# Optimization experiments

Measured on AMD Instinct MI355X. Metric: run time of the kernel, lower is better.

The kernel has to match this reference:

```python
import jax, jax.numpy as jnp
import numpy as np

N = 32768          # flattened vectors
HALF = 256         # each input half
D = 512            # embedding_dim
K = 2048           # num_embeddings
COMMITMENT_COST = 0.25


def setup_inputs() -> dict:
    key = jax.random.key(0)
    k0, k1, kw, kb, ke = jax.random.split(key, 5)
    x0 = jax.random.normal(k0, (N, HALF), dtype=jnp.float32)
    x1 = jax.random.normal(k1, (N, HALF), dtype=jnp.float32)
    # pre_lin: nn.Linear(D, D) -> weight [D, D], bias [D]
    lim = 1.0 / np.sqrt(D)
    W = jax.random.uniform(kw, (D, D), minval=-lim, maxval=lim, dtype=jnp.float32)
    b = jax.random.uniform(kb, (D,), minval=-lim, maxval=lim, dtype=jnp.float32)
    # codebook: embedding.weight.data.normal_()
    emb = jax.random.normal(ke, (K, D), dtype=jnp.float32)
    return {"x0": x0, "x1": x1, "W": W, "b": b, "emb": emb}


def reference(x0, x1, W, b, emb):
    # hstack the two halves -> [N, D]
    inputs = jnp.concatenate([x0, x1], axis=1)
    h = inputs @ W.T + b                       # pre_lin, [N, D]
    # squared L2 distances to codebook, [N, K]
    d2 = (jnp.sum(h * h, axis=1, keepdims=True)
          + jnp.sum(emb * emb, axis=1)
          - 2.0 * (h @ emb.T))
    idx = jnp.argmin(d2, axis=1)               # [N]
    encodings = jax.nn.one_hot(idx, emb.shape[0], dtype=jnp.float32)  # [N, K]
    quantized = emb[idx]                       # gather == one_hot @ emb, [N, D]
    # commitment loss (eval mode: no EMA update)
    e_latent_loss = jnp.mean((jax.lax.stop_gradient(quantized) - h) ** 2)
    loss = COMMITMENT_COST * e_latent_loss
    # straight-through estimator
    q_st = h + jax.lax.stop_gradient(quantized - h)
    avg_probs = jnp.mean(encodings, axis=0)
    perplexity = jnp.exp(-jnp.sum(avg_probs * jnp.log(avg_probs + 1e-10)))
    # row-major reshape [N, D] -> [2, N, D/2], as in torch.reshape
    q_out = jnp.reshape(q_st, (2, q_st.shape[0], -1))
    return loss, q_out, perplexity, encodings
```

## Files before the change

kernel.cpp:

```cpp
#include <hip/hip_runtime.h>
#include <cfloat>
#include <cmath>

#define NROWS 32768
#define DDIM  512
#define KCODES 2048

#define OUT_Q    1
#define OUT_PERP 16777217
#define OUT_ENC  16777218

#define AP_OFF    16777216
#define BP_OFF    33554432
#define XS_OFF    34603008
#define WS_OFF    51380224
#define ENORM_OFF 51642368
#define PVAL_OFF  51644416
#define PSEC_OFF  52692992
#define PIDX_OFF  53741568
#define AG_OFF    54790144
#define PVAL2_OFF 63178752
#define PSEC2_OFF 63703040
#define PIDX2_OFF 64227328
#define RB_OFF    64751616
#define RI_OFF    64784384

#define CAP1 16384
#define CAP2 4096
#define EPS1 0.32f
#define EPS2 0.02f

typedef __attribute__((ext_vector_type(8))) short  bf16x8;
typedef __attribute__((ext_vector_type(4))) float  f32x4;

__device__ __forceinline__ unsigned short f2bf(float f) {
  unsigned u = __float_as_uint(f);
  unsigned r = (u + 0x7FFF + ((u >> 16) & 1)) >> 16;
  return (unsigned short)r;
}
__device__ __forceinline__ float bf2f(unsigned short h) {
  return __uint_as_float(((unsigned)h) << 16);
}
__device__ __forceinline__ void gload16(const void* g, void* l) {
  __builtin_amdgcn_global_load_lds(
      (const __attribute__((address_space(1))) unsigned int*)g,
      (__attribute__((address_space(3))) unsigned int*)l, 16, 0, 0);
}
__device__ __forceinline__ ushort4 hi4(float4 v) {
  return make_ushort4(f2bf(v.x), f2bf(v.y), f2bf(v.z), f2bf(v.w));
}
__device__ __forceinline__ ushort4 lo4(float4 v, ushort4 h) {
  return make_ushort4(f2bf(v.x - bf2f(h.x)), f2bf(v.y - bf2f(h.y)),
                      f2bf(v.z - bf2f(h.z)), f2bf(v.w - bf2f(h.w)));
}

template<int TERMS, int KSTEPS>
__device__ __forceinline__ void kloop64(const unsigned short* __restrict__ Am,
    const unsigned short* __restrict__ Bm, short* Asm, short* Bsm,
    f32x4 (&acc)[4][4], int t, int wr, int wc, int lr, int lg) {
  for (int kt = 0; kt < KSTEPS; ++kt) {
    const int ph = kt >> 3, r64 = (kt & 7) * 64;
    int koffA, koffB;
    if (TERMS == 1)      { koffA = r64;                          koffB = r64; }
    else if (TERMS == 3) { koffA = (ph == 1) ? 512 + r64 : r64;  koffB = (ph == 2) ? 512 + r64 : r64; }
    else                 { koffA = (ph & 1) ? 512 + r64 : r64;   koffB = (ph & 2) ? 512 + r64 : r64; }
    const unsigned short* Agp = Am + koffA;
    const unsigned short* Bgp = Bm + koffB;
#pragma unroll
    for (int i = 0; i < 4; ++i) {
      const int chunk = i * 256 + t;
      const int r = chunk >> 3;
      const int c8s = (chunk & 7) ^ (r & 7);
      gload16(Agp + (size_t)r * 1024 + c8s * 8, Asm + chunk * 8);
      gload16(Bgp + (size_t)r * 1024 + c8s * 8, Bsm + chunk * 8);
    }
    __syncthreads();
#pragma unroll
    for (int kk = 0; kk < 2; ++kk) {
      const int xk = (kk * 32 + lg * 8) ^ ((lr & 7) << 3);
      bf16x8 a[4], b[4];
#pragma unroll
      for (int mi = 0; mi < 4; ++mi)
        a[mi] = *(const bf16x8*)&Asm[(wr * 64 + mi * 16 + lr) * 64 + xk];
#pragma unroll
      for (int ni = 0; ni < 4; ++ni)
        b[ni] = *(const bf16x8*)&Bsm[(wc * 64 + ni * 16 + lr) * 64 + xk];
#pragma unroll
      for (int mi = 0; mi < 4; ++mi)
#pragma unroll
        for (int ni = 0; ni < 4; ++ni)
          acc[mi][ni] = __builtin_amdgcn_mfma_f32_16x16x32_bf16(a[mi], b[ni], acc[mi][ni], 0, 0, 0);
    }
    __syncthreads();
  }
}

__global__ __launch_bounds__(256) void kprep_x(const float* __restrict__ x0,
    const float* __restrict__ x1, const float* __restrict__ W,
    unsigned short* __restrict__ Xs, unsigned short* __restrict__ Ws,
    unsigned int* __restrict__ wsclr) {
  if (blockIdx.x == 16640) {
    for (int i = threadIdx.x; i < 2052; i += 256) wsclr[i] = 0u;
    return;
  }
  const int i = blockIdx.x * 256 + threadIdx.x;
  if (i < 4194304) {
    const int half = i >> 21;
    const int j = i & 2097151;
    const int n = j >> 6;
    const int c4 = (j & 63) * 4;
    const float* src = half ? x1 : x0;
    const float4 v = *(const float4*)&src[(size_t)n * 256 + c4];
    const ushort4 hh = hi4(v);
    unsigned short* row = Xs + (size_t)n * 1024 + half * 256;
    *(ushort4*)&row[c4]       = hh;
    *(ushort4*)&row[512 + c4] = lo4(v, hh);
  } else {
    const int j = i - 4194304;
    const int r = j >> 7;
    const int c4 = (j & 127) * 4;
    const float4 v = *(const float4*)&W[(size_t)r * 512 + c4];
    const ushort4 hh = hi4(v);
    unsigned short* row = Ws + (size_t)r * 1024;
    *(ushort4*)&row[c4]       = hh;
    *(ushort4*)&row[512 + c4] = lo4(v, hh);
  }
}

__global__ __launch_bounds__(256) void kprep_emb(const float* __restrict__ emb,
    unsigned short* __restrict__ Bp, float* __restrict__ enorms) {
  __shared__ float part[4];
  const int t = threadIdx.x;
  const int row = blockIdx.x * 2 + (t >> 7);
  const int c4 = (t & 127) * 4;
  const float4 v = *(const float4*)&emb[(size_t)row * 512 + c4];
  const ushort4 hh = hi4(v);
  unsigned short* brow = Bp + (size_t)row * 1024;
  *(ushort4*)&brow[c4]       = hh;
  *(ushort4*)&brow[512 + c4] = lo4(v, hh);
  float s = v.x * v.x + v.y * v.y + v.z * v.z + v.w * v.w;
#pragma unroll
  for (int off = 32; off > 0; off >>= 1) s += __shfl_down(s, off);
  if ((t & 63) == 0) part[t >> 6] = s;
  __syncthreads();
  if (t == 0)   enorms[row] = part[0] + part[1];
  if (t == 128) enorms[row] = part[2] + part[3];
}

__global__ __launch_bounds__(256) void kgemm1_mfma(
    const unsigned short* __restrict__ Xs, const unsigned short* __restrict__ Ws,
    const float* __restrict__ bias, unsigned short* __restrict__ Ap) {
  __shared__ short Asm[128 * 64];
  __shared__ short Bsm[128 * 64];
  const int bid = blockIdx.x;
  const int n = (bid >> 3) & 3;
  const int m = (bid & 7) * 32 + (bid >> 5);
  const int m0 = m * 128, j0 = n * 128;
  const int t = threadIdx.x;
  const int wid = t >> 6, wr = wid >> 1, wc = wid & 1;
  const int lr = t & 15, lg = (t >> 4) & 3;

  f32x4 acc[4][4];
#pragma unroll
  for (int mi = 0; mi < 4; ++mi)
#pragma unroll
    for (int ni = 0; ni < 4; ++ni) acc[mi][ni] = (f32x4){0.f, 0.f, 0.f, 0.f};

  kloop64<4, 32>(Xs + (size_t)m0 * 1024, Ws + (size_t)j0 * 1024,
                 Asm, Bsm, acc, t, wr, wc, lr, lg);

#pragma unroll
  for (int ni = 0; ni < 4; ++ni) {
    const int col = j0 + wc * 64 + ni * 16 + lr;
    const float bb = bias[col];
#pragma unroll
    for (int mi = 0; mi < 4; ++mi)
#pragma unroll
      for (int jj = 0; jj < 4; ++jj) {
        const int row = m0 + wr * 64 + mi * 16 + lg * 4 + jj;
        const float v = acc[mi][ni][jj] + bb;
        const unsigned short hb = f2bf(v);
        Ap[(size_t)row * 1024 + col]       = hb;
        Ap[(size_t)row * 1024 + 512 + col] = f2bf(v - bf2f(hb));
      }
  }
}

template<int TERMS, bool GATED>
__global__ __launch_bounds__(256) void kdist_t(
    const unsigned short* __restrict__ A, const unsigned short* __restrict__ B,
    const float* __restrict__ enorms, float* __restrict__ pval,
    float* __restrict__ psec, int* __restrict__ pidx,
    const int* __restrict__ nflag, int mrows) {
  __shared__ short Asm[128 * 64];
  __shared__ short Bsm[128 * 64];
  const int bid = blockIdx.x;
  int m, n;
  if (GATED) {
    m = bid >> 4;
    n = bid & 15;
    const int nf = min(*nflag, CAP1);
    if (m >= ((nf + 127) >> 7)) return;
  } else {
    m = (bid & 7) * 32 + (bid >> 7);
    n = (bid >> 3) & 15;
  }
  const int m0 = m * 128;
  const int n0 = n * 128;
  const int t = threadIdx.x;
  const int wid = t >> 6, wr = wid >> 1, wc = wid & 1;
  const int lr = t & 15, lg = (t >> 4) & 3;

  f32x4 acc[4][4];
#pragma unroll
  for (int mi = 0; mi < 4; ++mi)
#pragma unroll
    for (int ni = 0; ni < 4; ++ni) acc[mi][ni] = (f32x4){0.f, 0.f, 0.f, 0.f};

  kloop64<TERMS, TERMS * 8>(A + (size_t)m0 * 1024, B + (size_t)n0 * 1024,
                            Asm, Bsm, acc, t, wr, wc, lr, lg);

  float en[4]; int kb[4];
#pragma unroll
  for (int ni = 0; ni < 4; ++ni) {
    kb[ni] = n0 + wc * 64 + ni * 16 + lr;
    en[ni] = enorms[kb[ni]];
  }
  const int p = n * 2 + wc;
#pragma unroll
  for (int mi = 0; mi < 4; ++mi)
#pragma unroll
    for (int j = 0; j < 4; ++j) {
      float bv = fmaf(-2.f, acc[mi][0][j], en[0]);
      int bk = kb[0];
      float sv = FLT_MAX;
#pragma unroll
      for (int ni = 1; ni < 4; ++ni) {
        const float v = fmaf(-2.f, acc[mi][ni][j], en[ni]);
        if (v < bv) { sv = bv; bv = v; bk = kb[ni]; }
        else sv = fminf(sv, v);
      }
#pragma unroll
      for (int msk = 1; msk < 16; msk <<= 1) {
        const float ob = __shfl_xor(bv, msk);
        const int   ok = __shfl_xor(bk, msk);
        const float os = __shfl_xor(sv, msk);
        if (ob < bv || (ob == bv && ok < bk)) { sv = fminf(bv, os); bv = ob; bk = ok; }
        else sv = fminf(sv, ob);
      }
      if (lr == 0) {
        const int row = m0 + wr * 64 + mi * 16 + lg * 4 + j;
        pval[(size_t)p * mrows + row] = bv;
        psec[(size_t)p * mrows + row] = sv;
        pidx[(size_t)p * mrows + row] = bk;
      }
    }
}

__global__ __launch_bounds__(256) void kreduce(const float* __restrict__ pval,
    const float* __restrict__ psec, const int* __restrict__ pidx,
    int* __restrict__ idx, int* __restrict__ nflag, int* __restrict__ flags) {
  const int r = blockIdx.x * 256 + threadIdx.x;
  float bv = FLT_MAX, sv = FLT_MAX;
  int bk = 0;
#pragma unroll
  for (int p = 0; p < 32; ++p) {
    const float v1 = pval[p * NROWS + r];
    const int   k1 = pidx[p * NROWS + r];
    const float s1 = psec[p * NROWS + r];
    if (v1 < bv || (v1 == bv && k1 < bk)) { sv = fminf(bv, s1); bv = v1; bk = k1; }
    else sv = fminf(sv, v1);
  }
  idx[r] = bk;
  if (sv - bv < EPS1) {
    const int pos = atomicAdd(nflag, 1);
    if (pos < CAP1) flags[pos] = r;
  }
}

__global__ __launch_bounds__(256) void kgather(const unsigned short* __restrict__ Ap,
    const int* __restrict__ flags, const int* __restrict__ nflag,
    unsigned short* __restrict__ Ag) {
  const int nf = min(*nflag, CAP1);
  const int t = threadIdx.x;
  const int g8 = blockIdx.x;
  for (int i = t; i < 8 * 256; i += 256) {
    const int rr = i >> 8;
    const int g = g8 * 8 + rr;
    if (g < nf) {
      const int c = i & 255;
      ((ushort4*)(Ag + (size_t)g * 1024))[c] =
          ((const ushort4*)(Ap + (size_t)flags[g] * 1024))[c];
    }
  }
}

__global__ __launch_bounds__(256) void kreduce2(const float* __restrict__ pval2,
    const float* __restrict__ psec2, const int* __restrict__ pidx2,
    const int* __restrict__ flags, const int* __restrict__ nflag,
    int* __restrict__ idx, int* __restrict__ nflag2, int* __restrict__ flags2) {
  const int nf = min(*nflag, CAP1);
  const int g = blockIdx.x * 256 + threadIdx.x;
  if (g >= nf) return;
  float bv = FLT_MAX, sv = FLT_MAX;
  int bk = 0;
#pragma unroll
  for (int p = 0; p < 32; ++p) {
    const float v1 = pval2[p * CAP1 + g];
    const int   k1 = pidx2[p * CAP1 + g];
    const float s1 = psec2[p * CAP1 + g];
    if (v1 < bv || (v1 == bv && k1 < bk)) { sv = fminf(bv, s1); bv = v1; bk = k1; }
    else sv = fminf(sv, v1);
  }
  const int r = flags[g];
  if (sv - bv >= EPS2) {
    idx[r] = bk;
  } else {
    const int pos = atomicAdd(nflag2, 1);
    if (pos < CAP2) flags2[pos] = r;
  }
}

__global__ __launch_bounds__(256) void krescore_p(
    const unsigned short* __restrict__ Ap, const float* __restrict__ emb,
    const float* __restrict__ enorms, const int* __restrict__ flags2,
    const int* __restrict__ nflag2, float* __restrict__ rbest,
    int* __restrict__ rbidx) {
  const int nf2 = min(*nflag2, CAP2);
  const int g2 = blockIdx.x >> 3;
  if (g2 >= nf2) return;
  const int chunk = blockIdx.x & 7;
  const int t = threadIdx.x;
  const int r = flags2[g2];
  __shared__ float hr[512];
  __shared__ float rv[256];
  __shared__ int   rk[256];
  for (int i = t; i < 128; i += 256) {
    const ushort4 hh = *(const ushort4*)&Ap[(size_t)r * 1024 + i * 4];
    const ushort4 ll = *(const ushort4*)&Ap[(size_t)r * 1024 + 512 + i * 4];
    hr[i * 4 + 0] = bf2f(hh.x) + bf2f(ll.x);
    hr[i * 4 + 1] = bf2f(hh.y) + bf2f(ll.y);
    hr[i * 4 + 2] = bf2f(hh.z) + bf2f(ll.z);
    hr[i * 4 + 3] = bf2f(hh.w) + bf2f(ll.w);
  }
  __syncthreads();
  const int c = chunk * 256 + t;
  const float* er = emb + (size_t)c * 512;
  float d0 = 0.f, d1 = 0.f, d2 = 0.f, d3 = 0.f;
#pragma unroll 8
  for (int dd = 0; dd < 512; dd += 16) {
    const float4 e0 = *(const float4*)&er[dd];
    const float4 e1 = *(const float4*)&er[dd + 4];
    const float4 e2 = *(const float4*)&er[dd + 8];
    const float4 e3 = *(const float4*)&er[dd + 12];
    d0 = fmaf(hr[dd+0],  e0.x, d0); d0 = fmaf(hr[dd+1],  e0.y, d0);
    d0 = fmaf(hr[dd+2],  e0.z, d0); d0 = fmaf(hr[dd+3],  e0.w, d0);
    d1 = fmaf(hr[dd+4],  e1.x, d1); d1 = fmaf(hr[dd+5],  e1.y, d1);
    d1 = fmaf(hr[dd+6],  e1.z, d1); d1 = fmaf(hr[dd+7],  e1.w, d1);
    d2 = fmaf(hr[dd+8],  e2.x, d2); d2 = fmaf(hr[dd+9],  e2.y, d2);
    d2 = fmaf(hr[dd+10], e2.z, d2); d2 = fmaf(hr[dd+11], e2.w, d2);
    d3 = fmaf(hr[dd+12], e3.x, d3); d3 = fmaf(hr[dd+13], e3.y, d3);
    d3 = fmaf(hr[dd+14], e3.z, d3); d3 = fmaf(hr[dd+15], e3.w, d3);
  }
  const float dot = (d0 + d1) + (d2 + d3);
  rv[t] = fmaf(-2.f, dot, enorms[c]);
  rk[t] = c;
  __syncthreads();
  for (int off = 128; off > 0; off >>= 1) {
    if (t < off) {
      const float v2 = rv[t + off];
      const int   k2 = rk[t + off];
      if (v2 < rv[t] || (v2 == rv[t] && k2 < rk[t])) { rv[t] = v2; rk[t] = k2; }
    }
    __syncthreads();
  }
  if (t == 0) {
    rbest[g2 * 8 + chunk] = rv[0];
    rbidx[g2 * 8 + chunk] = rk[0];
  }
}

__global__ __launch_bounds__(256) void kpick(const float* __restrict__ rbest,
    const int* __restrict__ rbidx, const int* __restrict__ flags2,
    const int* __restrict__ nflag2, int* __restrict__ idx) {
  const int g2 = blockIdx.x * 256 + threadIdx.x;
  if (g2 >= min(*nflag2, CAP2)) return;
  float bv = rbest[g2 * 8];
  int   bk = rbidx[g2 * 8];
#pragma unroll
  for (int c = 1; c < 8; ++c) {
    const float v = rbest[g2 * 8 + c];
    const int   k = rbidx[g2 * 8 + c];
    if (v < bv || (v == bv && k < bk)) { bv = v; bk = k; }
  }
  idx[flags2[g2]] = bk;
}

__global__ __launch_bounds__(256) void kquant(const unsigned short* __restrict__ Ap,
    const float* __restrict__ emb, const int* __restrict__ idx,
    float* __restrict__ qout, double* __restrict__ partials,
    int* __restrict__ counts) {
  const int t = threadIdx.x;
  const int base = blockIdx.x * 256 + t;
  float ls = 0.f;
#pragma unroll
  for (int i = 0; i < 8; ++i) {
    const int f4 = base + i * 524288;
    const int n  = f4 >> 7;
    const int c4 = (f4 & 127) << 2;
    const int in = idx[n];
    const ushort4 hh = *(const ushort4*)&Ap[(size_t)n * 1024 + c4];
    const ushort4 ll = *(const ushort4*)&Ap[(size_t)n * 1024 + 512 + c4];
    const float hx = bf2f(hh.x) + bf2f(ll.x);
    const float hy = bf2f(hh.y) + bf2f(ll.y);
    const float hz = bf2f(hh.z) + bf2f(ll.z);
    const float hw = bf2f(hh.w) + bf2f(ll.w);
    const float4 ev = *(const float4*)&emb[(size_t)in * DDIM + c4];
    f32x4 q;
    q.x = hx + (ev.x - hx);
    q.y = hy + (ev.y - hy);
    q.z = hz + (ev.z - hz);
    q.w = hw + (ev.w - hw);
    __builtin_nontemporal_store(q, (f32x4*)&qout[(size_t)f4 * 4]);
    const float dx = ev.x - hx, dy = ev.y - hy;
    const float dz = ev.z - hz, dw = ev.w - hw;
    ls += dx * dx + dy * dy + dz * dz + dw * dw;
    if (c4 == 0) atomicAdd(&counts[in], 1);
  }
  double s = (double)ls;
#pragma unroll
  for (int off = 32; off > 0; off >>= 1) s += __shfl_down(s, off);
  __shared__ double sred[4];
  if ((t & 63) == 0) sred[t >> 6] = s;
  __syncthreads();
  if (t == 0)
    partials[blockIdx.x] = sred[0] + sred[1] + sred[2] + sred[3];
}

__global__ __launch_bounds__(256) void kenc(const int* __restrict__ idx,
                                            float* __restrict__ outf) {
  const int tid = blockIdx.x * 256 + threadIdx.x;
#pragma unroll
  for (int j = 0; j < 4; ++j) {
    const int f4 = tid + j * 4194304;
    const int n  = f4 >> 9;
    const int k4 = (f4 & 511) << 2;
    const int in = idx[n];
    f32x4 v = {0.f, 0.f, 0.f, 0.f};
    if ((in & ~3) == k4) v[in & 3] = 1.f;
    __builtin_nontemporal_store(v, (f32x4*)&outf[(size_t)f4 * 4]);
  }
}

__global__ __launch_bounds__(256) void kfinal(const double* __restrict__ partials,
    const int* __restrict__ counts, float* __restrict__ out) {
  __shared__ double sred[256];
  const int t = threadIdx.x;
  double s = 0.0;
  for (int k = t; k < 2048; k += 256) s += partials[k];
  sred[t] = s;
  __syncthreads();
  for (int off = 128; off > 0; off >>= 1) {
    if (t < off) sred[t] += sred[t + off];
    __syncthreads();
  }
  const double loss_sum = sred[0];
  __syncthreads();
  double e = 0.0;
  for (int k = t; k < KCODES; k += 256) {
    const double p = counts[k] / 32768.0;
    e += p * log(p + 1e-10);
  }
  sred[t] = e;
  __syncthreads();
  for (int off = 128; off > 0; off >>= 1) {
    if (t < off) sred[t] += sred[t + off];
    __syncthreads();
  }
  if (t == 0) {
    out[0]        = (float)(0.25 * loss_sum / (32768.0 * 512.0));
    out[OUT_PERP] = (float)exp(-sred[0]);
  }
}

extern "C" void kernel_launch(void* const* d_in, const int* in_sizes, int n_in,
                              void* d_out, int out_size, void* d_ws, size_t ws_size,
                              hipStream_t stream) {
  const float* x0  = (const float*)d_in[0];
  const float* x1  = (const float*)d_in[1];
  const float* W   = (const float*)d_in[2];
  const float* b   = (const float*)d_in[3];
  const float* emb = (const float*)d_in[4];
  float* out = (float*)d_out;
  float* S   = out + OUT_ENC + 2;

  unsigned short* Ap = (unsigned short*)(S + AP_OFF);
  unsigned short* Bp = (unsigned short*)(S + BP_OFF);
  unsigned short* Xs = (unsigned short*)(S + XS_OFF);
  unsigned short* Ws = (unsigned short*)(S + WS_OFF);
  unsigned short* Ag = (unsigned short*)(S + AG_OFF);
  int* pidx  = (int*)(S + PIDX_OFF);
  int* pidx2 = (int*)(S + PIDX2_OFF);
  int* rbidx = (int*)(S + RI_OFF);

  int* nflag  = (int*)((char*)d_ws + 8);
  int* nflag2 = (int*)((char*)d_ws + 12);
  int* counts = (int*)((char*)d_ws + 16);
  int* idx    = (int*)((char*)d_ws + 8208);
  int* flags  = (int*)((char*)d_ws + 139280);
  int* flags2 = (int*)((char*)d_ws + 204816);
  double* partials = (double*)((char*)d_ws + 221200);

  kprep_x<<<16641, 256, 0, stream>>>(x0, x1, W, Xs, Ws, (unsigned int*)d_ws);
  kprep_emb<<<1024, 256, 0, stream>>>(emb, Bp, S + ENORM_OFF);
  kgemm1_mfma<<<1024, 256, 0, stream>>>(Xs, Ws, b, Ap);
  kdist_t<1, false><<<4096, 256, 0, stream>>>(Ap, Bp, S + ENORM_OFF,
      S + PVAL_OFF, S + PSEC_OFF, pidx, nflag, NROWS);
  kreduce<<<128, 256, 0, stream>>>(S + PVAL_OFF, S + PSEC_OFF, pidx, idx, nflag, flags);
  kgather<<<2048, 256, 0, stream>>>(Ap, flags, nflag, Ag);
  kdist_t<3, true><<<2048, 256, 0, stream>>>(Ag, Bp, S + ENORM_OFF,
      S + PVAL2_OFF, S + PSEC2_OFF, pidx2, nflag, CAP1);
  kreduce2<<<64, 256, 0, stream>>>(S + PVAL2_OFF, S + PSEC2_OFF, pidx2,
                                   flags, nflag, idx, nflag2, flags2);
  krescore_p<<<CAP2 * 8, 256, 0, stream>>>(Ap, emb, S + ENORM_OFF,
      flags2, nflag2, S + RB_OFF, rbidx);
  kpick<<<16, 256, 0, stream>>>(S + RB_OFF, rbidx, flags2, nflag2, idx);
  kquant<<<2048, 256, 0, stream>>>(Ap, emb, idx, out + OUT_Q, partials, counts);
  kenc<<<16384, 256, 0, stream>>>(idx, out + OUT_ENC);
  kfinal<<<1, 256, 0, stream>>>(partials, counts, out);
}
```

Measured before the change: 485.8 us.

## Fuse gather into gated distance GEMM and merge prep kernels

The separate gather kernel that copied flagged rows of Ap into a contiguous buffer is removed. The gated second-pass distance kernel now reads rows indirectly through the flags array by precomputing per-thread row offsets. The two prep kernels are also merged into one launch to save a kernel launch. The gain is less memory traffic and fewer launches. The cost is scattered A-tile loads in the gated GEMM, which may coalesce less well than loads from a contiguous buffer.

```diff
diff --git a/kernel.cpp b/kernel.cpp
--- a/kernel.cpp
+++ b/kernel.cpp
@@ -18,7 +18,6 @@
 #define PVAL_OFF  51644416
 #define PSEC_OFF  52692992
 #define PIDX_OFF  53741568
-#define AG_OFF    54790144
 #define PVAL2_OFF 63178752
 #define PSEC2_OFF 63703040
 #define PIDX2_OFF 64227328
@@ -55,23 +54,23 @@
 }
 
 template<int TERMS, int KSTEPS>
-__device__ __forceinline__ void kloop64(const unsigned short* __restrict__ Am,
-    const unsigned short* __restrict__ Bm, short* Asm, short* Bsm,
-    f32x4 (&acc)[4][4], int t, int wr, int wc, int lr, int lg) {
+__device__ __forceinline__ void kloop64(const unsigned short* __restrict__ Abase,
+    const unsigned short* __restrict__ Bm, const size_t* __restrict__ arow,
+    short* Asm, short* Bsm, f32x4 (&acc)[4][4],
+    int t, int wr, int wc, int lr, int lg) {
   for (int kt = 0; kt < KSTEPS; ++kt) {
     const int ph = kt >> 3, r64 = (kt & 7) * 64;
     int koffA, koffB;
     if (TERMS == 1)      { koffA = r64;                          koffB = r64; }
     else if (TERMS == 3) { koffA = (ph == 1) ? 512 + r64 : r64;  koffB = (ph == 2) ? 512 + r64 : r64; }
     else                 { koffA = (ph & 1) ? 512 + r64 : r64;   koffB = (ph & 2) ? 512 + r64 : r64; }
-    const unsigned short* Agp = Am + koffA;
     const unsigned short* Bgp = Bm + koffB;
 #pragma unroll
     for (int i = 0; i < 4; ++i) {
       const int chunk = i * 256 + t;
       const int r = chunk >> 3;
       const int c8s = (chunk & 7) ^ (r & 7);
-      gload16(Agp + (size_t)r * 1024 + c8s * 8, Asm + chunk * 8);
+      gload16(Abase + arow[i] + koffA + c8s * 8, Asm + chunk * 8);
       gload16(Bgp + (size_t)r * 1024 + c8s * 8, Bsm + chunk * 8);
     }
     __syncthreads();
@@ -95,16 +94,15 @@
   }
 }
 
-__global__ __launch_bounds__(256) void kprep_x(const float* __restrict__ x0,
+__global__ __launch_bounds__(256) void kprep(const float* __restrict__ x0,
     const float* __restrict__ x1, const float* __restrict__ W,
-    unsigned short* __restrict__ Xs, unsigned short* __restrict__ Ws,
-    unsigned int* __restrict__ wsclr) {
-  if (blockIdx.x == 16640) {
-    for (int i = threadIdx.x; i < 2052; i += 256) wsclr[i] = 0u;
-    return;
-  }
-  const int i = blockIdx.x * 256 + threadIdx.x;
-  if (i < 4194304) {
+    const float* __restrict__ emb, unsigned short* __restrict__ Xs,
+    unsigned short* __restrict__ Ws, unsigned short* __restrict__ Bp,
+    float* __restrict__ enorms, unsigned int* __restrict__ wsclr) {
+  const int bid = blockIdx.x;
+  const int t = threadIdx.x;
+  if (bid < 16384) {
+    const int i = bid * 256 + t;
     const int half = i >> 21;
     const int j = i & 2097151;
     const int n = j >> 6;
@@ -115,8 +113,8 @@
     unsigned short* row = Xs + (size_t)n * 1024 + half * 256;
     *(ushort4*)&row[c4]       = hh;
     *(ushort4*)&row[512 + c4] = lo4(v, hh);
-  } else {
-    const int j = i - 4194304;
+  } else if (bid < 16640) {
+    const int j = (bid - 16384) * 256 + t;
     const int r = j >> 7;
     const int c4 = (j & 127) * 4;
     const float4 v = *(const float4*)&W[(size_t)r * 512 + c4];
@@ -124,27 +122,25 @@
     unsigned short* row = Ws + (size_t)r * 1024;
     *(ushort4*)&row[c4]       = hh;
     *(ushort4*)&row[512 + c4] = lo4(v, hh);
-  }
-}
-
-__global__ __launch_bounds__(256) void kprep_emb(const float* __restrict__ emb,
-    unsigned short* __restrict__ Bp, float* __restrict__ enorms) {
-  __shared__ float part[4];
-  const int t = threadIdx.x;
-  const int row = blockIdx.x * 2 + (t >> 7);
-  const int c4 = (t & 127) * 4;
-  const float4 v = *(const float4*)&emb[(size_t)row * 512 + c4];
-  const ushort4 hh = hi4(v);
-  unsigned short* brow = Bp + (size_t)row * 1024;
-  *(ushort4*)&brow[c4]       = hh;
-  *(ushort4*)&brow[512 + c4] = lo4(v, hh);
-  float s = v.x * v.x + v.y * v.y + v.z * v.z + v.w * v.w;
-#pragma unroll
-  for (int off = 32; off > 0; off >>= 1) s += __shfl_down(s, off);
-  if ((t & 63) == 0) part[t >> 6] = s;
-  __syncthreads();
-  if (t == 0)   enorms[row] = part[0] + part[1];
-  if (t == 128) enorms[row] = part[2] + part[3];
+  } else if (bid == 16640) {
+    for (int i = t; i < 2052; i += 256) wsclr[i] = 0u;
+  } else {
+    __shared__ float part[4];
+    const int row = (bid - 16641) * 2 + (t >> 7);
+    const int c4 = (t & 127) * 4;
+    const float4 v = *(const float4*)&emb[(size_t)row * 512 + c4];
+    const ushort4 hh = hi4(v);
+    unsigned short* brow = Bp + (size_t)row * 1024;
+    *(ushort4*)&brow[c4]       = hh;
+    *(ushort4*)&brow[512 + c4] = lo4(v, hh);
+    float s = v.x * v.x + v.y * v.y + v.z * v.z + v.w * v.w;
+#pragma unroll
+    for (int off = 32; off > 0; off >>= 1) s += __shfl_down(s, off);
+    if ((t & 63) == 0) part[t >> 6] = s;
+    __syncthreads();
+    if (t == 0)   enorms[row] = part[0] + part[1];
+    if (t == 128) enorms[row] = part[2] + part[3];
+  }
 }
 
 __global__ __launch_bounds__(256) void kgemm1_mfma(
@@ -159,6 +155,10 @@
   const int t = threadIdx.x;
   const int wid = t >> 6, wr = wid >> 1, wc = wid & 1;
   const int lr = t & 15, lg = (t >> 4) & 3;
+  size_t arow[4];
+#pragma unroll
+  for (int i = 0; i < 4; ++i)
+    arow[i] = (size_t)(m0 + i * 32 + (t >> 3)) * 1024;
 
   f32x4 acc[4][4];
 #pragma unroll
@@ -166,8 +166,7 @@
 #pragma unroll
     for (int ni = 0; ni < 4; ++ni) acc[mi][ni] = (f32x4){0.f, 0.f, 0.f, 0.f};
 
-  kloop64<4, 32>(Xs + (size_t)m0 * 1024, Ws + (size_t)j0 * 1024,
-                 Asm, Bsm, acc, t, wr, wc, lr, lg);
+  kloop64<4, 32>(Xs, Ws + (size_t)j0 * 1024, arow, Asm, Bsm, acc, t, wr, wc, lr, lg);
 
 #pragma unroll
   for (int ni = 0; ni < 4; ++ni) {
@@ -191,15 +190,15 @@
     const unsigned short* __restrict__ A, const unsigned short* __restrict__ B,
     const float* __restrict__ enorms, float* __restrict__ pval,
     float* __restrict__ psec, int* __restrict__ pidx,
-    const int* __restrict__ nflag, int mrows) {
+    const int* __restrict__ nflag, const int* __restrict__ flags, int mrows) {
   __shared__ short Asm[128 * 64];
   __shared__ short Bsm[128 * 64];
   const int bid = blockIdx.x;
-  int m, n;
+  int m, n, nf = 0;
   if (GATED) {
     m = bid >> 4;
     n = bid & 15;
-    const int nf = min(*nflag, CAP1);
+    nf = min(*nflag, CAP1);
     if (m >= ((nf + 127) >> 7)) return;
   } else {
     m = (bid & 7) * 32 + (bid >> 7);
@@ -210,6 +209,13 @@
   const int t = threadIdx.x;
   const int wid = t >> 6, wr = wid >> 1, wc = wid & 1;
   const int lr = t & 15, lg = (t >> 4) & 3;
+  size_t arow[4];
+#pragma unroll
+  for (int i = 0; i < 4; ++i) {
+    const int g = m0 + i * 32 + (t >> 3);
+    const int src = GATED ? flags[g < nf ? g : nf - 1] : g;
+    arow[i] = (size_t)src * 1024;
+  }
 
   f32x4 acc[4][4];
 #pragma unroll
@@ -217,8 +223,8 @@
 #pragma unroll
     for (int ni = 0; ni < 4; ++ni) acc[mi][ni] = (f32x4){0.f, 0.f, 0.f, 0.f};
 
-  kloop64<TERMS, TERMS * 8>(A + (size_t)m0 * 1024, B + (size_t)n0 * 1024,
-                            Asm, Bsm, acc, t, wr, wc, lr, lg);
+  kloop64<TERMS, TERMS * 8>(A, B + (size_t)n0 * 1024, arow, Asm, Bsm, acc,
+                            t, wr, wc, lr, lg);
 
   float en[4]; int kb[4];
 #pragma unroll
@@ -275,23 +281,6 @@
   if (sv - bv < EPS1) {
     const int pos = atomicAdd(nflag, 1);
     if (pos < CAP1) flags[pos] = r;
-  }
-}
-
-__global__ __launch_bounds__(256) void kgather(const unsigned short* __restrict__ Ap,
-    const int* __restrict__ flags, const int* __restrict__ nflag,
-    unsigned short* __restrict__ Ag) {
-  const int nf = min(*nflag, CAP1);
-  const int t = threadIdx.x;
-  const int g8 = blockIdx.x;
-  for (int i = t; i < 8 * 256; i += 256) {
-    const int rr = i >> 8;
-    const int g = g8 * 8 + rr;
-    if (g < nf) {
-      const int c = i & 255;
-      ((ushort4*)(Ag + (size_t)g * 1024))[c] =
-          ((const ushort4*)(Ap + (size_t)flags[g] * 1024))[c];
-    }
   }
 }
 
@@ -498,7 +487,6 @@
   unsigned short* Bp = (unsigned short*)(S + BP_OFF);
   unsigned short* Xs = (unsigned short*)(S + XS_OFF);
   unsigned short* Ws = (unsigned short*)(S + WS_OFF);
-  unsigned short* Ag = (unsigned short*)(S + AG_OFF);
   int* pidx  = (int*)(S + PIDX_OFF);
   int* pidx2 = (int*)(S + PIDX2_OFF);
   int* rbidx = (int*)(S + RI_OFF);
@@ -511,15 +499,14 @@
   int* flags2 = (int*)((char*)d_ws + 204816);
   double* partials = (double*)((char*)d_ws + 221200);
 
-  kprep_x<<<16641, 256, 0, stream>>>(x0, x1, W, Xs, Ws, (unsigned int*)d_ws);
-  kprep_emb<<<1024, 256, 0, stream>>>(emb, Bp, S + ENORM_OFF);
+  kprep<<<17665, 256, 0, stream>>>(x0, x1, W, emb, Xs, Ws, Bp,
+                                   S + ENORM_OFF, (unsigned int*)d_ws);
   kgemm1_mfma<<<1024, 256, 0, stream>>>(Xs, Ws, b, Ap);
   kdist_t<1, false><<<4096, 256, 0, stream>>>(Ap, Bp, S + ENORM_OFF,
-      S + PVAL_OFF, S + PSEC_OFF, pidx, nflag, NROWS);
+      S + PVAL_OFF, S + PSEC_OFF, pidx, nflag, nullptr, NROWS);
   kreduce<<<128, 256, 0, stream>>>(S + PVAL_OFF, S + PSEC_OFF, pidx, idx, nflag, flags);
-  kgather<<<2048, 256, 0, stream>>>(Ap, flags, nflag, Ag);
-  kdist_t<3, true><<<2048, 256, 0, stream>>>(Ag, Bp, S + ENORM_OFF,
-      S + PVAL2_OFF, S + PSEC2_OFF, pidx2, nflag, CAP1);
+  kdist_t<3, true><<<2048, 256, 0, stream>>>(Ap, Bp, S + ENORM_OFF,
+      S + PVAL2_OFF, S + PSEC2_OFF, pidx2, nflag, flags, CAP1);
   kreduce2<<<64, 256, 0, stream>>>(S + PVAL2_OFF, S + PSEC2_OFF, pidx2,
                                    flags, nflag, idx, nflag2, flags2);
   krescore_p<<<CAP2 * 8, 256, 0, stream>>>(Ap, emb, S + ENORM_OFF,
```

New measurement: 477.4 us (median of 2 runs). About the same (-1.7%).
